# Kernel tuning notes

Measured on AMD Instinct MI355X. Metric: run time of the kernel, lower is better.

Reference implementation:

```python
import jax, jax.numpy as jnp
import numpy as np


def _grad(x, axis):
    """torch.gradient with unit spacing: central diff interior, one-sided edges."""
    def sl(a, b):
        idx = [slice(None)] * x.ndim
        idx[axis] = slice(a, b)
        return x[tuple(idx)]
    left = sl(1, 2) - sl(0, 1)                 # (x[1]-x[0])
    mid = (sl(2, None) - sl(0, -2)) * 0.5      # (x[i+1]-x[i-1])/2
    right = sl(-1, None) - sl(-2, -1)          # (x[-1]-x[-2])
    return jnp.concatenate([left, mid, right], axis=axis)


def _mse0(e):
    return jnp.mean(e * e)  # MSE against zeros


def _phy_loss(V_all, P_all, F_all, Re):
    Vy = V_all[:, :, :, :, 0, :]
    Vx = V_all[:, :, :, :, 1, :]
    Vz = V_all[:, :, :, :, 2, :]
    Fy = F_all[:, :, :, :, 0, :]
    Fx = F_all[:, :, :, :, 1, :]
    Fz = F_all[:, :, :, :, 2, :]
    # first derivatives (dims: 1=y, 2=x, 3=z, 4=t)
    dVydt, dVydy, dVydx, dVydz = _grad(Vy, 4), _grad(Vy, 1), _grad(Vy, 2), _grad(Vy, 3)
    dVxdt, dVxdy, dVxdx, dVxdz = _grad(Vx, 4), _grad(Vx, 1), _grad(Vx, 2), _grad(Vx, 3)
    dVzdt, dVzdy, dVzdx, dVzdz = _grad(Vz, 4), _grad(Vz, 1), _grad(Vz, 2), _grad(Vz, 3)
    dPdx, dPdy, dPdz = _grad(P_all, 2), _grad(P_all, 1), _grad(P_all, 3)
    # second derivatives
    lapVx = _grad(dVxdx, 2) + _grad(dVxdy, 1) + _grad(dVxdz, 3)
    lapVy = _grad(dVydx, 2) + _grad(dVydy, 1) + _grad(dVydz, 3)
    lapVz = _grad(dVzdx, 2) + _grad(dVzdy, 1) + _grad(dVzdz, 3)
    e1 = dVydt + (Vx * dVydx + Vy * dVydy + Vz * dVydz + dPdy) - Re * lapVy + Fy
    e2 = dVxdt + (Vx * dVxdx + Vy * dVxdy + Vz * dVxdz + dPdx) - Re * lapVx + Fx
    e3 = dVzdt + (Vx * dVzdx + Vy * dVzdy + Vz * dVzdz + dPdz) - Re * lapVz + Fz
    e4 = dVxdx + dVydy + dVzdz
    return _mse0(e1) + _mse0(e2) + _mse0(e3) + _mse0(e4)


def _time_loss(C_all, Y_data, X_last):
    Y_last = jnp.concatenate([X_last, Y_data[:, :, :, :, :-1]], axis=4)
    t1 = jnp.mean((Y_last - Y_data) ** 2)
    t2 = jnp.mean((C_all - Y_data) ** 2)
    return jnp.where(jax.lax.stop_gradient(t1) < jax.lax.stop_gradient(t2), t2 - t1, 0.0)


def setup_inputs() -> dict:
    key = jax.random.key(0)
    ks = jax.random.split(key, 9)
    B, S, T = 2, 48, 16
    f = jnp.float32
    return {
        "C_all": jax.random.normal(ks[0], (B, S, S, S, T), f),
        "V_all": jax.random.normal(ks[1], (B, S, S, S, 3, T), f),
        "P_all": jax.random.normal(ks[2], (B, S, S, S, T), f),
        "X_all": jax.random.normal(ks[3], (B, S, S, S, T), f),
        "X1_all": jax.random.normal(ks[4], (B, S, S, S, T), f),
        "F_all": jax.random.normal(ks[5], (B, S, S, S, 3, T), f),
        "Re": jnp.ones((1,), f),
        "X_last": jax.random.normal(ks[6], (B, S, S, S, 1), f),
        "Y_data": jax.random.normal(ks[7], (B, S, S, S, T), f),
        "maskd0": jnp.ones((1,), f),
        "maskd1": jnp.ones((1,), f),
        "maskd2": jnp.ones((1,), f),
    }


def reference(C_all, V_all, P_all, X_all, X1_all, F_all, Re, X_last, Y_data, maskd0, maskd1, maskd2):
    main1 = jnp.mean((X1_all - Y_data) ** 2)
    main2 = jnp.mean((X_all - Y_data) ** 2)
    phy = _phy_loss(V_all, P_all, F_all, Re)
    tl = _time_loss(C_all, Y_data, X_last)
    return (main1, main2, phy, tl)
```

## Files before the change

### kernel.cpp

```cpp
#include <hip/hip_runtime.h>

#define S 48
#define T 16
#define NTOT (2 * S * S * S * T)
#define NC (NTOT / 4)
#define NBLK 1152

__device__ __forceinline__ float4 ld4(const float* p) {
    return *reinterpret_cast<const float4*>(p);
}
__device__ __forceinline__ float4 operator-(float4 a, float4 b) {
    return make_float4(a.x - b.x, a.y - b.y, a.z - b.z, a.w - b.w);
}
__device__ __forceinline__ float4 operator+(float4 a, float4 b) {
    return make_float4(a.x + b.x, a.y + b.y, a.z + b.z, a.w + b.w);
}
__device__ __forceinline__ float4 operator*(float s, float4 a) {
    return make_float4(s * a.x, s * a.y, s * a.z, s * a.w);
}
__device__ __forceinline__ float4 operator*(float4 a, float4 b) {
    return make_float4(a.x * b.x, a.y * b.y, a.z * b.z, a.w * b.w);
}
__device__ __forceinline__ float sum2(float4 a) {
    return a.x * a.x + a.y * a.y + a.z * a.z + a.w * a.w;
}

struct AxisP {
    int om2, om1, op1, op2;
    float w, cm2, cm1, cc, cp1, cp2;
};
__device__ __forceinline__ AxisP axis_params(int i, int N) {
    AxisP a;
    a.om1 = (i > 0) ? -1 : 0;
    a.op1 = (i < N - 1) ? 1 : 0;
    a.om2 = (i >= 2) ? -2 : 0;
    a.op2 = (i < N - 2) ? 2 : 0;
    a.w   = (i > 0 && i < N - 1) ? 0.5f : 1.0f;
    a.cm2 = (i < 2) ? 0.0f : ((i == N - 1) ? 0.5f : 0.25f);
    a.cm1 = (i == 1) ? 0.5f : ((i == N - 1) ? -1.0f : 0.0f);
    a.cc  = (i == 0) ? 0.5f : (i == 1 || i == N - 2) ? -0.75f : (i == N - 1) ? 0.5f : -0.5f;
    a.cp1 = (i == 0) ? -1.0f : ((i == N - 2) ? 0.5f : 0.0f);
    a.cp2 = (i == 0) ? 0.5f : (i == 1) ? 0.25f : (i < N - 2) ? 0.25f : 0.0f;
    return a;
}

__device__ __forceinline__ void gboth(const float* __restrict__ fc, float4 c,
                                      const AxisP& a, int stride,
                                      float4& g1, float4& g2) {
    const float4 m2 = ld4(fc + a.om2 * stride);
    const float4 m1 = ld4(fc + a.om1 * stride);
    const float4 p1 = ld4(fc + a.op1 * stride);
    const float4 p2 = ld4(fc + a.op2 * stride);
    g1 = a.w * (p1 - m1);
    g2 = a.cm2 * m2 + a.cm1 * m1 + a.cc * c + a.cp1 * p1 + a.cp2 * p2;
}

__device__ __forceinline__ float4 d1t(float4 c, const float* __restrict__ fc, int t0) {
    float4 r;
    r.x = (t0 == 0) ? (c.y - c.x) : (c.y - fc[-1]) * 0.5f;
    r.y = (c.z - c.x) * 0.5f;
    r.z = (c.w - c.y) * 0.5f;
    r.w = (t0 == 12) ? (c.w - c.z) : (fc[4] - c.z) * 0.5f;
    return r;
}

__global__ __launch_bounds__(256) void fused_loss(
    const float* __restrict__ Cmat, const float* __restrict__ V,
    const float* __restrict__ P, const float* __restrict__ Xa,
    const float* __restrict__ X1a, const float* __restrict__ F,
    const float* __restrict__ Rep, const float* __restrict__ Xlast,
    const float* __restrict__ Y, float* __restrict__ ws)
{
    const float re = Rep[0];
    float am1 = 0.f, am2 = 0.f, aphy = 0.f, at1 = 0.f, at2 = 0.f;

    for (int n4 = blockIdx.x * 256 + threadIdx.x; n4 < NC; n4 += NBLK * 256) {
        const int sp = n4 >> 2;
        const int t0 = (n4 & 3) << 2;
        const int z  = sp % S;
        const int r1 = sp / S;
        const int x  = r1 % S;
        const int y  = (r1 / S) % S;

        const AxisP az = axis_params(z, S);
        const AxisP ax = axis_params(x, S);
        const AxisP ay = axis_params(y, S);

        const int prow = sp * T + t0;
        const float4 yv  = ld4(Y + prow);
        const float4 x1v = ld4(X1a + prow);
        const float4 xv  = ld4(Xa + prow);
        const float4 cvv = ld4(Cmat + prow);
        am1 += sum2(x1v - yv);
        am2 += sum2(xv - yv);
        at2 += sum2(cvv - yv);
        const float yp0 = (t0 == 0) ? Xlast[sp] : Y[prow - 1];
        at1 += sum2(make_float4(yp0, yv.x, yv.y, yv.z) - yv);

        const float* Pc = P + prow;
        const float4 dPdz = az.w * (ld4(Pc + az.op1 * 16)    - ld4(Pc + az.om1 * 16));
        const float4 dPdx = ax.w * (ld4(Pc + ax.op1 * 768)   - ld4(Pc + ax.om1 * 768));
        const float4 dPdy = ay.w * (ld4(Pc + ay.op1 * 36864) - ld4(Pc + ay.om1 * 36864));

        const int vbase = sp * 48 + t0;
        const float* Vyc = V + vbase;
        const float* Vxc = V + vbase + 16;
        const float* Vzc = V + vbase + 32;
        const float4 vy = ld4(Vyc), vx = ld4(Vxc), vz = ld4(Vzc);
        const float4 fy = ld4(F + vbase), fx = ld4(F + vbase + 16), fz = ld4(F + vbase + 32);

        float4 e4 = make_float4(0.f, 0.f, 0.f, 0.f);

        {
            float4 dz, lz, dx_, lx, dy_, ly;
            gboth(Vyc, vy, az, 48, dz, lz);
            gboth(Vyc, vy, ax, 2304, dx_, lx);
            gboth(Vyc, vy, ay, 110592, dy_, ly);
            const float4 dt = d1t(vy, Vyc, t0);
            const float4 lap = lz + lx + ly;
            const float4 e = dt + vx * dx_ + vy * dy_ + vz * dz + dPdy + (-re) * lap + fy;
            aphy += sum2(e);
            e4 = e4 + dy_;
        }
        {
            float4 dz, lz, dx_, lx, dy_, ly;
            gboth(Vxc, vx, az, 48, dz, lz);
            gboth(Vxc, vx, ax, 2304, dx_, lx);
            gboth(Vxc, vx, ay, 110592, dy_, ly);
            const float4 dt = d1t(vx, Vxc, t0);
            const float4 lap = lz + lx + ly;
            const float4 e = dt + vx * dx_ + vy * dy_ + vz * dz + dPdx + (-re) * lap + fx;
            aphy += sum2(e);
            e4 = e4 + dx_;
        }
        {
            float4 dz, lz, dx_, lx, dy_, ly;
            gboth(Vzc, vz, az, 48, dz, lz);
            gboth(Vzc, vz, ax, 2304, dx_, lx);
            gboth(Vzc, vz, ay, 110592, dy_, ly);
            const float4 dt = d1t(vz, Vzc, t0);
            const float4 lap = lz + lx + ly;
            const float4 e = dt + vx * dx_ + vy * dy_ + vz * dz + dPdz + (-re) * lap + fz;
            aphy += sum2(e);
            e4 = e4 + dz;
        }
        aphy += sum2(e4);
    }

    #pragma unroll
    for (int off = 32; off > 0; off >>= 1) {
        am1  += __shfl_down(am1, off);
        am2  += __shfl_down(am2, off);
        aphy += __shfl_down(aphy, off);
        at1  += __shfl_down(at1, off);
        at2  += __shfl_down(at2, off);
    }
    __shared__ float sred[4][5];
    const int lane = threadIdx.x & 63;
    const int wv   = threadIdx.x >> 6;
    if (lane == 0) {
        sred[wv][0] = am1; sred[wv][1] = am2; sred[wv][2] = aphy;
        sred[wv][3] = at1; sred[wv][4] = at2;
    }
    __syncthreads();
    if (threadIdx.x == 0) {
        float s0 = 0.f, s1 = 0.f, s2 = 0.f, s3 = 0.f, s4 = 0.f;
        #pragma unroll
        for (int w = 0; w < 4; ++w) {
            s0 += sred[w][0]; s1 += sred[w][1]; s2 += sred[w][2];
            s3 += sred[w][3]; s4 += sred[w][4];
        }
        atomicAdd(&ws[0], s0);
        atomicAdd(&ws[1], s1);
        atomicAdd(&ws[2], s2);
        atomicAdd(&ws[3], s3);
        atomicAdd(&ws[4], s4);
    }
}

__global__ void finalize_kernel(const float* __restrict__ ws, float* __restrict__ out) {
    const float invN = 1.0f / (float)NTOT;
    const float m1  = ws[0] * invN;
    const float m2  = ws[1] * invN;
    const float phy = ws[2] * invN;
    const float t1  = ws[3] * invN;
    const float t2  = ws[4] * invN;
    out[0] = m1;
    out[1] = m2;
    out[2] = phy;
    out[3] = (t1 < t2) ? (t2 - t1) : 0.0f;
}

extern "C" void kernel_launch(void* const* d_in, const int* in_sizes, int n_in,
                              void* d_out, int out_size, void* d_ws, size_t ws_size,
                              hipStream_t stream) {
    const float* Cmat  = (const float*)d_in[0];
    const float* V     = (const float*)d_in[1];
    const float* P     = (const float*)d_in[2];
    const float* Xa    = (const float*)d_in[3];
    const float* X1a   = (const float*)d_in[4];
    const float* F     = (const float*)d_in[5];
    const float* Rep   = (const float*)d_in[6];
    const float* Xlast = (const float*)d_in[7];
    const float* Y     = (const float*)d_in[8];

    float* ws  = (float*)d_ws;
    float* out = (float*)d_out;

    hipMemsetAsync(ws, 0, 5 * sizeof(float), stream);
    fused_loss<<<NBLK, 256, 0, stream>>>(Cmat, V, P, Xa, X1a, F, Rep, Xlast, Y, ws);
    finalize_kernel<<<1, 1, 0, stream>>>(ws, out);
}
```

Before: 275.7 us.

## Map one block per (x,y,b) z-line instead of grid-stride loop

Replaces the 1152-block grid-stride loop with a 3D grid of 48x48x2 blocks of 192 threads, where each thread handles one (z, t-quad) of a single x-y column. Index math becomes block-derived, which removes the per-element div/mod work. F loads are moved next to their use to shorten register live ranges, and launch bounds of (192, 4) are set. The cost is 4608 blocks, each doing its own atomicAdd reduction, so global atomic traffic and block launch overhead go up.

```diff
diff --git a/kernel.cpp b/kernel.cpp
--- a/kernel.cpp
+++ b/kernel.cpp
@@ -3,8 +3,7 @@
 #define S 48
 #define T 16
 #define NTOT (2 * S * S * S * T)
-#define NC (NTOT / 4)
-#define NBLK 1152
+
 
 __device__ __forceinline__ float4 ld4(const float* p) {
     return *reinterpret_cast<const float4*>(p);
@@ -64,50 +63,51 @@
     return r;
 }
 
-__global__ __launch_bounds__(256) void fused_loss(
+__global__ __launch_bounds__(192, 4) void fused_loss(
     const float* __restrict__ Cmat, const float* __restrict__ V,
     const float* __restrict__ P, const float* __restrict__ Xa,
     const float* __restrict__ X1a, const float* __restrict__ F,
     const float* __restrict__ Rep, const float* __restrict__ Xlast,
     const float* __restrict__ Y, float* __restrict__ ws)
 {
+    const int x = blockIdx.x, y = blockIdx.y, b = blockIdx.z;
+    const int tid = threadIdx.x;
+    const int z  = tid >> 2;
+    const int t0 = (tid & 3) << 2;
+
     const float re = Rep[0];
-    float am1 = 0.f, am2 = 0.f, aphy = 0.f, at1 = 0.f, at2 = 0.f;
-
-    for (int n4 = blockIdx.x * 256 + threadIdx.x; n4 < NC; n4 += NBLK * 256) {
-        const int sp = n4 >> 2;
-        const int t0 = (n4 & 3) << 2;
-        const int z  = sp % S;
-        const int r1 = sp / S;
-        const int x  = r1 % S;
-        const int y  = (r1 / S) % S;
-
-        const AxisP az = axis_params(z, S);
-        const AxisP ax = axis_params(x, S);
-        const AxisP ay = axis_params(y, S);
-
-        const int prow = sp * T + t0;
+
+    const AxisP az = axis_params(z, S);
+    const AxisP ax = axis_params(x, S);
+    const AxisP ay = axis_params(y, S);
+
+    const int base_p = b * 1769472 + y * 36864 + x * 768;
+    const int base_v = b * 5308416 + y * 110592 + x * 2304;
+    const int sp     = ((b * S + y) * S + x) * S + z;
+
+    float am1, am2, aphy = 0.f, at1, at2;
+    {
+        const int prow = base_p + 4 * tid;
+
         const float4 yv  = ld4(Y + prow);
         const float4 x1v = ld4(X1a + prow);
         const float4 xv  = ld4(Xa + prow);
         const float4 cvv = ld4(Cmat + prow);
-        am1 += sum2(x1v - yv);
-        am2 += sum2(xv - yv);
-        at2 += sum2(cvv - yv);
+        am1 = sum2(x1v - yv);
+        am2 = sum2(xv - yv);
+        at2 = sum2(cvv - yv);
         const float yp0 = (t0 == 0) ? Xlast[sp] : Y[prow - 1];
-        at1 += sum2(make_float4(yp0, yv.x, yv.y, yv.z) - yv);
+        at1 = sum2(make_float4(yp0, yv.x, yv.y, yv.z) - yv);
 
         const float* Pc = P + prow;
         const float4 dPdz = az.w * (ld4(Pc + az.op1 * 16)    - ld4(Pc + az.om1 * 16));
         const float4 dPdx = ax.w * (ld4(Pc + ax.op1 * 768)   - ld4(Pc + ax.om1 * 768));
         const float4 dPdy = ay.w * (ld4(Pc + ay.op1 * 36864) - ld4(Pc + ay.om1 * 36864));
 
-        const int vbase = sp * 48 + t0;
-        const float* Vyc = V + vbase;
-        const float* Vxc = V + vbase + 16;
-        const float* Vzc = V + vbase + 32;
+        const float* Vyc = V + base_v + z * 48 + t0;
+        const float* Vxc = Vyc + 16;
+        const float* Vzc = Vyc + 32;
         const float4 vy = ld4(Vyc), vx = ld4(Vxc), vz = ld4(Vzc);
-        const float4 fy = ld4(F + vbase), fx = ld4(F + vbase + 16), fz = ld4(F + vbase + 32);
 
         float4 e4 = make_float4(0.f, 0.f, 0.f, 0.f);
 
@@ -117,8 +117,9 @@
             gboth(Vyc, vy, ax, 2304, dx_, lx);
             gboth(Vyc, vy, ay, 110592, dy_, ly);
             const float4 dt = d1t(vy, Vyc, t0);
-            const float4 lap = lz + lx + ly;
-            const float4 e = dt + vx * dx_ + vy * dy_ + vz * dz + dPdy + (-re) * lap + fy;
+            const float4 fy = ld4(F + base_v + z * 48 + t0);
+            const float4 e = dt + vx * dx_ + vy * dy_ + vz * dz + dPdy
+                             + (-re) * (lz + lx + ly) + fy;
             aphy += sum2(e);
             e4 = e4 + dy_;
         }
@@ -128,8 +129,9 @@
             gboth(Vxc, vx, ax, 2304, dx_, lx);
             gboth(Vxc, vx, ay, 110592, dy_, ly);
             const float4 dt = d1t(vx, Vxc, t0);
-            const float4 lap = lz + lx + ly;
-            const float4 e = dt + vx * dx_ + vy * dy_ + vz * dz + dPdx + (-re) * lap + fx;
+            const float4 fx = ld4(F + base_v + z * 48 + t0 + 16);
+            const float4 e = dt + vx * dx_ + vy * dy_ + vz * dz + dPdx
+                             + (-re) * (lz + lx + ly) + fx;
             aphy += sum2(e);
             e4 = e4 + dx_;
         }
@@ -139,8 +141,9 @@
             gboth(Vzc, vz, ax, 2304, dx_, lx);
             gboth(Vzc, vz, ay, 110592, dy_, ly);
             const float4 dt = d1t(vz, Vzc, t0);
-            const float4 lap = lz + lx + ly;
-            const float4 e = dt + vx * dx_ + vy * dy_ + vz * dz + dPdz + (-re) * lap + fz;
+            const float4 fz = ld4(F + base_v + z * 48 + t0 + 32);
+            const float4 e = dt + vx * dx_ + vy * dy_ + vz * dz + dPdz
+                             + (-re) * (lz + lx + ly) + fz;
             aphy += sum2(e);
             e4 = e4 + dz;
         }
@@ -155,18 +158,18 @@
         at1  += __shfl_down(at1, off);
         at2  += __shfl_down(at2, off);
     }
-    __shared__ float sred[4][5];
-    const int lane = threadIdx.x & 63;
-    const int wv   = threadIdx.x >> 6;
+    __shared__ float sred[3][5];
+    const int lane = tid & 63;
+    const int wv   = tid >> 6;
     if (lane == 0) {
         sred[wv][0] = am1; sred[wv][1] = am2; sred[wv][2] = aphy;
         sred[wv][3] = at1; sred[wv][4] = at2;
     }
     __syncthreads();
-    if (threadIdx.x == 0) {
+    if (tid == 0) {
         float s0 = 0.f, s1 = 0.f, s2 = 0.f, s3 = 0.f, s4 = 0.f;
         #pragma unroll
-        for (int w = 0; w < 4; ++w) {
+        for (int w = 0; w < 3; ++w) {
             s0 += sred[w][0]; s1 += sred[w][1]; s2 += sred[w][2];
             s3 += sred[w][3]; s4 += sred[w][4];
         }
@@ -208,6 +211,7 @@
     float* out = (float*)d_out;
 
     hipMemsetAsync(ws, 0, 5 * sizeof(float), stream);
-    fused_loss<<<NBLK, 256, 0, stream>>>(Cmat, V, P, Xa, X1a, F, Rep, Xlast, Y, ws);
+    dim3 grid(S, S, 2);
+    fused_loss<<<grid, 192, 0, stream>>>(Cmat, V, P, Xa, X1a, F, Rep, Xlast, Y, ws);
     finalize_kernel<<<1, 1, 0, stream>>>(ws, out);
 }
```

Measured after the change: 504.5 us. 83.0% more time.
